# Kernel tuning notes

Hardware: AMD Instinct MI355X
Metric: run time of the kernel (lower is better)

## Reference

```python
import jax, jax.numpy as jnp
import numpy as np

OUT_NPOINT = 1024
NSAMPLE = 64
RADIUS = 0.32
BN_EPS = 1e-5


def _fps_single(pts, npoint):
    # pts: [N,3] -> indices [npoint], sequential furthest point sampling (starts at index 0,
    # matching pointnet2's furthest_point_sample with dists initialized to 1e10).
    N = pts.shape[0]

    def step(carry, _):
        mind, last = carry
        d = jnp.sum((pts - pts[last]) ** 2, axis=-1)  # [N]
        mind = jnp.minimum(mind, d)
        nxt = jnp.argmax(mind).astype(jnp.int32)
        return (mind, nxt), last

    init = (jnp.full((N,), 1e10, dtype=pts.dtype), jnp.int32(0))
    (_, _), idxs = jax.lax.scan(step, init, None, length=npoint)
    return idxs  # [npoint]


def _ball_query(xyz, new_xyz, radius, nsample):
    # xyz: [B,N,3], new_xyz: [B,M,3] -> idx [B,M,nsample] (first nsample in-ball points,
    # padded with the first found index, matching pointnet2 ball_query semantics).
    N = xyz.shape[1]
    d2 = jnp.sum((new_xyz[:, :, None, :] - xyz[:, None, :, :]) ** 2, axis=-1)  # [B,M,N]
    inball = d2 < radius * radius
    key = jnp.where(inball, jnp.arange(N, dtype=jnp.int32)[None, None, :], jnp.int32(N))
    sorted_keys = jnp.sort(key, axis=-1)[..., :nsample]  # [B,M,nsample]
    valid = sorted_keys < N
    first = jnp.where(sorted_keys[..., 0:1] < N, sorted_keys[..., 0:1], 0)
    return jnp.where(valid, sorted_keys, first)


def _group(features, idx):
    # features: [B,C,N], idx: [B,M,S] -> [B,C,M,S]
    return jax.vmap(lambda f, i: f[:, i])(features, idx)


def setup_inputs() -> dict:
    key = jax.random.key(0)
    ks = jax.random.split(key, 8)
    B, N, Cin, Cout = 8, 4096, 128, 256
    xyz = jax.random.uniform(ks[0], (B, N, 3), dtype=jnp.float32)
    features = jax.random.normal(ks[1], (B, Cin, N), dtype=jnp.float32)
    W = jax.random.normal(ks[2], (Cout, Cin), dtype=jnp.float32) * 0.05  # 1x1 conv weight
    b = jax.random.normal(ks[3], (Cout,), dtype=jnp.float32) * 0.05
    gamma = jax.random.uniform(ks[4], (Cout,), minval=0.5, maxval=1.5, dtype=jnp.float32)
    beta = jax.random.normal(ks[5], (Cout,), dtype=jnp.float32) * 0.1
    run_mean = jax.random.normal(ks[6], (Cout,), dtype=jnp.float32) * 0.1
    run_var = jax.random.uniform(ks[7], (Cout,), minval=0.5, maxval=1.5, dtype=jnp.float32)
    return {"xyz": xyz, "features": features, "W": W, "b": b,
            "gamma": gamma, "beta": beta, "run_mean": run_mean, "run_var": run_var}


def reference(xyz, features, W, b, gamma, beta, run_mean, run_var):
    # FPS to pick OUT_NPOINT centers
    fps_idx = jax.vmap(lambda p: _fps_single(p, OUT_NPOINT))(xyz)          # [B,M]
    new_xyz = jnp.take_along_axis(xyz, fps_idx[:, :, None], axis=1)        # [B,M,3]
    # ball-query neighbor indices and gather features (use_xyz=False)
    idx = _ball_query(xyz, new_xyz, RADIUS, NSAMPLE)                        # [B,M,S]
    grouped = _group(features, idx)                                         # [B,Cin,M,S]
    # pointwise conv (1x1) + BN (inference mode) + ReLU
    out = jnp.einsum('oc,bcms->boms', W, grouped) + b[None, :, None, None]  # [B,Cout,M,S]
    inv = jax.lax.rsqrt(run_var + BN_EPS)
    out = (out - run_mean[None, :, None, None]) * (gamma * inv)[None, :, None, None] + beta[None, :, None, None]
    out = jax.nn.relu(out)
    # max-pool over the neighbor axis
    return jnp.max(out, axis=-1)  # [B,Cout,M]
```

## Files before the change

kernel.cpp:

```cpp
#include <hip/hip_runtime.h>

#define N_PTS 4096
#define B_SZ  8
#define M_OUT 1024
#define NS    64
#define CIN   128
#define COUT  256
#define NW    496

typedef float v2f __attribute__((ext_vector_type(2)));

__device__ __forceinline__ float dpp_max_f32(float v) {
  int x = __builtin_bit_cast(int, v);
#define STG(C)                                                              \
  {                                                                         \
    int y = __builtin_amdgcn_update_dpp(x, x, C, 0xF, 0xF, false);          \
    float a = __builtin_bit_cast(float, x);                                 \
    float b2 = __builtin_bit_cast(float, y);                                \
    a = fmaxf(a, b2);                                                       \
    x = __builtin_bit_cast(int, a);                                         \
  }
  STG(0x111) STG(0x112) STG(0x114) STG(0x118) STG(0x142) STG(0x143)
#undef STG
  return __builtin_bit_cast(float, __builtin_amdgcn_readlane(x, 63));
}

__global__ __launch_bounds__(256) void fused_kernel(
    const float* __restrict__ xyz, int* __restrict__ fps_idx,
    int* __restrict__ gdone, const float* __restrict__ F,
    const float* __restrict__ W, float* __restrict__ Z,
    const float* __restrict__ bias, const float* __restrict__ gamma,
    const float* __restrict__ beta, const float* __restrict__ rmean,
    const float* __restrict__ rvar, float* __restrict__ out) {
  __shared__ __align__(16) float smem[13360];
  if (blockIdx.x < 8) {
#pragma clang fp contract(off)
    __builtin_amdgcn_s_setprio(3);
    float* lx = smem;
    float* ly = smem + 4096;
    float* lz = smem + 8192;
    float4 (*sl)[4] = (float4(*)[4])(smem + 12288);
    int (*siw)[4] = (int(*)[4])(smem + 12320);
    const int b = blockIdx.x, t = threadIdx.x;
    const int lane = t & 63, wv = t >> 6;
    const float* base = xyz + b * N_PTS * 3;
    for (int e = t; e < N_PTS; e += 256) {
      lx[e] = base[e * 3 + 0];
      ly[e] = base[e * 3 + 1];
      lz[e] = base[e * 3 + 2];
    }
    __syncthreads();
    const int nb = t * 16;
    v2f px[8], py[8], pz[8], m2[8];
#pragma unroll
    for (int j = 0; j < 8; ++j) {
      int n0 = nb + 2 * j;
      px[j] = (v2f){lx[n0], lx[n0 + 1]};
      py[j] = (v2f){ly[n0], ly[n0 + 1]};
      pz[j] = (v2f){lz[n0], lz[n0 + 1]};
      m2[j] = (v2f){1e10f, 1e10f};
    }
    int cur = 0;
    float cx = lx[0], cy = ly[0], cz = lz[0];
    for (int i = 0; i < M_OUT; ++i) {
      if (t == 0)
        __hip_atomic_store(fps_idx + b * M_OUT + i, cur, __ATOMIC_RELAXED,
                           __HIP_MEMORY_SCOPE_AGENT);
      float bv = -1.0f;
      int bj = 0;
#pragma unroll
      for (int j = 0; j < 8; ++j) {
        v2f dx = px[j] - cx, dy = py[j] - cy, dz = pz[j] - cz;
        v2f d = dx * dx + dy * dy;
        d = d + dz * dz;
        v2f md = __builtin_elementwise_min(m2[j], d);
        m2[j] = md;
        if (md.x > bv) { bv = md.x; bj = 2 * j; }
        if (md.y > bv) { bv = md.y; bj = 2 * j + 1; }
      }
      const float mv = dpp_max_f32(bv);
      unsigned long long tied = __ballot(bv == mv);
      const int fl = __ffsll(tied) - 1;
      const int bi = nb + bj;
      const int widx = __builtin_amdgcn_readlane(bi, fl);
      const float wx = lx[widx], wy = ly[widx], wz = lz[widx];
      const int p = i & 1;
      if (lane == 0) {
        sl[p][wv] = make_float4(mv, wx, wy, wz);
        siw[p][wv] = widx;
      }
      __syncthreads();
      float4 s0 = sl[p][0], s1 = sl[p][1], s2 = sl[p][2], s3 = sl[p][3];
      int i0 = siw[p][0], i1 = siw[p][1], i2 = siw[p][2], i3 = siw[p][3];
      float gv = s0.x, gx = s0.y, gy = s0.z, gz = s0.w;
      int gi = i0;
      bool bt;
      bt = (s1.x > gv) || (s1.x == gv && i1 < gi);
      if (bt) { gv = s1.x; gi = i1; gx = s1.y; gy = s1.z; gz = s1.w; }
      bt = (s2.x > gv) || (s2.x == gv && i2 < gi);
      if (bt) { gv = s2.x; gi = i2; gx = s2.y; gy = s2.z; gz = s2.w; }
      bt = (s3.x > gv) || (s3.x == gv && i3 < gi);
      if (bt) { gv = s3.x; gi = i3; gx = s3.y; gy = s3.z; gz = s3.w; }
      cur = gi; cx = gx; cy = gy; cz = gz;
    }
  } else {
    const int w = blockIdx.x - 8;
    {
      float (*Bs)[68] = (float(*)[68])smem;
      float (*As)[68] = (float(*)[68])(smem + 8704);
      const int tid = threadIdx.x;
      const int tx = tid & 15, ty = tid >> 4;
      for (int tile = w; tile < 2048; tile += NW) {
        __syncthreads();
        const int n0 = (tile & 63) * 64;
        const int o0 = ((tile >> 6) & 3) * 64;
        const int bb = tile >> 8;
        for (int l = 0; l < 32; ++l) {
          int e = l * 256 + tid;
          int c = e & 127, oo = e >> 7;
          Bs[c][oo] = W[(o0 + oo) * CIN + c];
        }
        float acc[4][4] = {};
        const float* Fb = F + bb * CIN * N_PTS;
        for (int c0 = 0; c0 < CIN; c0 += 32) {
          __syncthreads();
          for (int l = 0; l < 8; ++l) {
            int e = l * 256 + tid;
            int nn = e & 63, cc = e >> 6;
            As[cc][nn] = Fb[(c0 + cc) * N_PTS + n0 + nn];
          }
          __syncthreads();
#pragma unroll
          for (int cc = 0; cc < 32; ++cc) {
            float4 a = *(const float4*)&As[cc][tx * 4];
            float4 w4 = *(const float4*)&Bs[c0 + cc][ty * 4];
            acc[0][0] += a.x * w4.x; acc[0][1] += a.x * w4.y; acc[0][2] += a.x * w4.z; acc[0][3] += a.x * w4.w;
            acc[1][0] += a.y * w4.x; acc[1][1] += a.y * w4.y; acc[1][2] += a.y * w4.z; acc[1][3] += a.y * w4.w;
            acc[2][0] += a.z * w4.x; acc[2][1] += a.z * w4.y; acc[2][2] += a.z * w4.z; acc[2][3] += a.z * w4.w;
            acc[3][0] += a.w * w4.x; acc[3][1] += a.w * w4.y; acc[3][2] += a.w * w4.z; acc[3][3] += a.w * w4.w;
          }
        }
        float* Zb = Z + (size_t)(bb * N_PTS + n0) * COUT + o0;
#pragma unroll
        for (int i2 = 0; i2 < 4; ++i2) {
          int nn = tx * 4 + i2;
          float4 v = make_float4(acc[i2][0], acc[i2][1], acc[i2][2], acc[i2][3]);
          *(float4*)&Zb[(size_t)nn * COUT + ty * 4] = v;
        }
      }
    }
    __syncthreads();
    if (threadIdx.x == 0)
      __hip_atomic_fetch_add(gdone, 1, __ATOMIC_RELEASE,
                             __HIP_MEMORY_SCOPE_AGENT);
    if (threadIdx.x == 0) {
      while (__hip_atomic_load(gdone, __ATOMIC_ACQUIRE,
                               __HIP_MEMORY_SCOPE_AGENT) < NW)
        __builtin_amdgcn_s_sleep(16);
    }
    __syncthreads();
    __builtin_amdgcn_fence(__ATOMIC_ACQUIRE, "agent");
    const int lane = threadIdx.x & 63, wv = threadIdx.x >> 6;
    const int o = threadIdx.x;
    const float sc = gamma[o] * (1.0f / sqrtf(rvar[o] + 1e-5f));
    const float bo = bias[o], mo = rmean[o], bt = beta[o];
    float (*T)[9] = (float(*)[9])smem;
    int* sidx = (int*)(smem + 2304);
    int* cctr = (int*)(smem + 2816);
    for (int tb = w; tb < 1024; tb += NW) {
      const int b = tb & 7;
      const int m0 = (tb >> 3) * 8;
      if (threadIdx.x == 0) {
        int got;
        do {
          got = 1;
#pragma unroll
          for (int c = 0; c < 8; ++c) {
            int v = __hip_atomic_load(fps_idx + b * M_OUT + m0 + c,
                                      __ATOMIC_RELAXED,
                                      __HIP_MEMORY_SCOPE_AGENT);
            cctr[c] = v;
            got &= (v != -1);
          }
          if (!got) __builtin_amdgcn_s_sleep(8);
        } while (!got);
      }
      __syncthreads();
      const float* base = xyz + b * N_PTS * 3;
      {
#pragma clang fp contract(off)
        for (int c = wv; c < 8; c += 4) {
          const int cidx = cctr[c];
          const float cx = base[cidx * 3 + 0], cy = base[cidx * 3 + 1],
                      cz = base[cidx * 3 + 2];
          int* srow = sidx + c * NS;
          int cnt = 0, first = 0;
          for (int ch = 0; ch < N_PTS / 64 && cnt < NS; ++ch) {
            const int n = ch * 64 + lane;
            float dx = base[n * 3 + 0] - cx;
            float dy = base[n * 3 + 1] - cy;
            float dz = base[n * 3 + 2] - cz;
            float d = dx * dx + dy * dy;
            d = d + dz * dz;
            const bool inb = d < 0.1024f;
            unsigned long long mask = __ballot(inb);
            if (cnt == 0 && mask) first = ch * 64 + (__ffsll(mask) - 1);
            const int pos = cnt + __popcll(mask & ((1ull << lane) - 1ull));
            if (inb && pos < NS) srow[pos] = n;
            cnt += (int)__popcll(mask);
          }
          if (lane >= cnt) srow[lane] = first;
        }
      }
      __syncthreads();
      const float* Zb = Z + (size_t)b * N_PTS * COUT;
      for (int mi = 0; mi < 8; ++mi) {
        float c0 = -1e30f, c1 = -1e30f, c2 = -1e30f, c3 = -1e30f;
        float c4 = -1e30f, c5 = -1e30f, c6 = -1e30f, c7 = -1e30f;
#pragma unroll
        for (int s = 0; s < NS; s += 8) {
          int4 iv0 = *(const int4*)&sidx[mi * NS + s];
          int4 iv1 = *(const int4*)&sidx[mi * NS + s + 4];
          c0 = fmaxf(c0, Zb[(size_t)iv0.x * COUT + o]);
          c1 = fmaxf(c1, Zb[(size_t)iv0.y * COUT + o]);
          c2 = fmaxf(c2, Zb[(size_t)iv0.z * COUT + o]);
          c3 = fmaxf(c3, Zb[(size_t)iv0.w * COUT + o]);
          c4 = fmaxf(c4, Zb[(size_t)iv1.x * COUT + o]);
          c5 = fmaxf(c5, Zb[(size_t)iv1.y * COUT + o]);
          c6 = fmaxf(c6, Zb[(size_t)iv1.z * COUT + o]);
          c7 = fmaxf(c7, Zb[(size_t)iv1.w * COUT + o]);
        }
        float best = fmaxf(fmaxf(fmaxf(c0, c1), fmaxf(c2, c3)),
                           fmaxf(fmaxf(c4, c5), fmaxf(c6, c7)));
        float tv = best + bo;
        tv = (tv - mo) * sc + bt;
        T[o][mi] = fmaxf(tv, 0.0f);
      }
      __syncthreads();
      for (int l = 0; l < 8; ++l) {
        int e = l * 256 + (int)threadIdx.x;
        int mm = e & 7, oo = e >> 3;
        out[(size_t)(b * COUT + oo) * M_OUT + m0 + mm] = T[oo][mm];
      }
    }
  }
}

extern "C" void kernel_launch(void* const* d_in, const int* in_sizes, int n_in,
                              void* d_out, int out_size, void* d_ws, size_t ws_size,
                              hipStream_t stream) {
  const float* xyz      = (const float*)d_in[0];
  const float* features = (const float*)d_in[1];
  const float* W        = (const float*)d_in[2];
  const float* bias     = (const float*)d_in[3];
  const float* gamma    = (const float*)d_in[4];
  const float* beta     = (const float*)d_in[5];
  const float* rmean    = (const float*)d_in[6];
  const float* rvar     = (const float*)d_in[7];
  float* out = (float*)d_out;

  char* ws = (char*)d_ws;
  int* fps   = (int*)ws;
  int* flags = (int*)(ws + (48 << 10));
  float* Z   = (float*)(ws + (64 << 10) + (2 << 20));

  hipMemsetAsync(fps, 0xFF, 32 << 10, stream);
  hipMemsetAsync(flags, 0, 64, stream);
  fused_kernel<<<8 + NW, 256, 0, stream>>>(
      xyz, fps, flags, features, W, Z, bias, gamma, beta, rmean, rvar, out);
}
```

Baseline: 812.5 us.

## Split tail FPS centers into single-center tiles and merge memsets

Groups covering the last 64 FPS centers per batch are handled as single-center work items instead of 8-center tiles, so the ball-query and max-pool tail can follow the serial FPS loop more closely and finish sooner after the last index is published. The FPS loop exits after storing the final index, skipping the unused last distance update. The two workspace memsets are merged into one by initialising the done counter to -1 and waiting for NW-1. The per-center tail items use only one wave for the ball query and write output uncoalesced, adding some work-item overhead.

Result: no change. 803.0 us (-1.2%).

```diff
diff --git a/kernel.cpp b/kernel.cpp
--- a/kernel.cpp
+++ b/kernel.cpp
@@ -7,6 +7,8 @@
 #define CIN   128
 #define COUT  256
 #define NW    496
+#define NTILE_N 960
+#define NTILE_T 1472
 
 typedef float v2f __attribute__((ext_vector_type(2)));
 
@@ -66,6 +68,7 @@
       if (t == 0)
         __hip_atomic_store(fps_idx + b * M_OUT + i, cur, __ATOMIC_RELAXED,
                            __HIP_MEMORY_SCOPE_AGENT);
+      if (i == M_OUT - 1) break;
       float bv = -1.0f;
       int bj = 0;
 #pragma unroll
@@ -155,7 +158,7 @@
                              __HIP_MEMORY_SCOPE_AGENT);
     if (threadIdx.x == 0) {
       while (__hip_atomic_load(gdone, __ATOMIC_ACQUIRE,
-                               __HIP_MEMORY_SCOPE_AGENT) < NW)
+                               __HIP_MEMORY_SCOPE_AGENT) < NW - 1)
         __builtin_amdgcn_s_sleep(16);
     }
     __syncthreads();
@@ -167,33 +170,101 @@
     float (*T)[9] = (float(*)[9])smem;
     int* sidx = (int*)(smem + 2304);
     int* cctr = (int*)(smem + 2816);
-    for (int tb = w; tb < 1024; tb += NW) {
-      const int b = tb & 7;
-      const int m0 = (tb >> 3) * 8;
-      if (threadIdx.x == 0) {
-        int got;
-        do {
-          got = 1;
-#pragma unroll
-          for (int c = 0; c < 8; ++c) {
-            int v = __hip_atomic_load(fps_idx + b * M_OUT + m0 + c,
-                                      __ATOMIC_RELAXED,
-                                      __HIP_MEMORY_SCOPE_AGENT);
-            cctr[c] = v;
-            got &= (v != -1);
-          }
-          if (!got) __builtin_amdgcn_s_sleep(8);
-        } while (!got);
-      }
-      __syncthreads();
-      const float* base = xyz + b * N_PTS * 3;
-      {
+    for (int tb = w; tb < NTILE_T; tb += NW) {
+      if (tb < NTILE_N) {
+        const int b = tb & 7;
+        const int m0 = (tb >> 3) * 8;
+        if (threadIdx.x == 0) {
+          int got;
+          do {
+            got = 1;
+#pragma unroll
+            for (int c = 0; c < 8; ++c) {
+              int v = __hip_atomic_load(fps_idx + b * M_OUT + m0 + c,
+                                        __ATOMIC_RELAXED,
+                                        __HIP_MEMORY_SCOPE_AGENT);
+              cctr[c] = v;
+              got &= (v != -1);
+            }
+            if (!got) __builtin_amdgcn_s_sleep(8);
+          } while (!got);
+        }
+        __syncthreads();
+        const float* base = xyz + b * N_PTS * 3;
+        {
 #pragma clang fp contract(off)
-        for (int c = wv; c < 8; c += 4) {
-          const int cidx = cctr[c];
+          for (int c = wv; c < 8; c += 4) {
+            const int cidx = cctr[c];
+            const float cx = base[cidx * 3 + 0], cy = base[cidx * 3 + 1],
+                        cz = base[cidx * 3 + 2];
+            int* srow = sidx + c * NS;
+            int cnt = 0, first = 0;
+            for (int ch = 0; ch < N_PTS / 64 && cnt < NS; ++ch) {
+              const int n = ch * 64 + lane;
+              float dx = base[n * 3 + 0] - cx;
+              float dy = base[n * 3 + 1] - cy;
+              float dz = base[n * 3 + 2] - cz;
+              float d = dx * dx + dy * dy;
+              d = d + dz * dz;
+              const bool inb = d < 0.1024f;
+              unsigned long long mask = __ballot(inb);
+              if (cnt == 0 && mask) first = ch * 64 + (__ffsll(mask) - 1);
+              const int pos = cnt + __popcll(mask & ((1ull << lane) - 1ull));
+              if (inb && pos < NS) srow[pos] = n;
+              cnt += (int)__popcll(mask);
+            }
+            if (lane >= cnt) srow[lane] = first;
+          }
+        }
+        __syncthreads();
+        const float* Zb = Z + (size_t)b * N_PTS * COUT;
+        for (int mi = 0; mi < 8; ++mi) {
+          float c0 = -1e30f, c1 = -1e30f, c2 = -1e30f, c3 = -1e30f;
+          float c4 = -1e30f, c5 = -1e30f, c6 = -1e30f, c7 = -1e30f;
+#pragma unroll
+          for (int s = 0; s < NS; s += 8) {
+            int4 iv0 = *(const int4*)&sidx[mi * NS + s];
+            int4 iv1 = *(const int4*)&sidx[mi * NS + s + 4];
+            c0 = fmaxf(c0, Zb[(size_t)iv0.x * COUT + o]);
+            c1 = fmaxf(c1, Zb[(size_t)iv0.y * COUT + o]);
+            c2 = fmaxf(c2, Zb[(size_t)iv0.z * COUT + o]);
+            c3 = fmaxf(c3, Zb[(size_t)iv0.w * COUT + o]);
+            c4 = fmaxf(c4, Zb[(size_t)iv1.x * COUT + o]);
+            c5 = fmaxf(c5, Zb[(size_t)iv1.y * COUT + o]);
+            c6 = fmaxf(c6, Zb[(size_t)iv1.z * COUT + o]);
+            c7 = fmaxf(c7, Zb[(size_t)iv1.w * COUT + o]);
+          }
+          float best = fmaxf(fmaxf(fmaxf(c0, c1), fmaxf(c2, c3)),
+                             fmaxf(fmaxf(c4, c5), fmaxf(c6, c7)));
+          float tv = best + bo;
+          tv = (tv - mo) * sc + bt;
+          T[o][mi] = fmaxf(tv, 0.0f);
+        }
+        __syncthreads();
+        for (int l = 0; l < 8; ++l) {
+          int e = l * 256 + (int)threadIdx.x;
+          int mm = e & 7, oo = e >> 3;
+          out[(size_t)(b * COUT + oo) * M_OUT + m0 + mm] = T[oo][mm];
+        }
+      } else {
+        const int k = tb - NTILE_N;
+        const int b = k & 7;
+        const int m = 960 + (k >> 3);
+        if (threadIdx.x == 0) {
+          int v;
+          while ((v = __hip_atomic_load(fps_idx + b * M_OUT + m,
+                                        __ATOMIC_RELAXED,
+                                        __HIP_MEMORY_SCOPE_AGENT)) == -1)
+            __builtin_amdgcn_s_sleep(2);
+          cctr[0] = v;
+        }
+        __syncthreads();
+        const float* base = xyz + b * N_PTS * 3;
+        if (wv == 0) {
+#pragma clang fp contract(off)
+          const int cidx = cctr[0];
           const float cx = base[cidx * 3 + 0], cy = base[cidx * 3 + 1],
                       cz = base[cidx * 3 + 2];
-          int* srow = sidx + c * NS;
           int cnt = 0, first = 0;
           for (int ch = 0; ch < N_PTS / 64 && cnt < NS; ++ch) {
             const int n = ch * 64 + lane;
@@ -206,21 +277,19 @@
             unsigned long long mask = __ballot(inb);
             if (cnt == 0 && mask) first = ch * 64 + (__ffsll(mask) - 1);
             const int pos = cnt + __popcll(mask & ((1ull << lane) - 1ull));
-            if (inb && pos < NS) srow[pos] = n;
+            if (inb && pos < NS) sidx[pos] = n;
             cnt += (int)__popcll(mask);
           }
-          if (lane >= cnt) srow[lane] = first;
-        }
-      }
-      __syncthreads();
-      const float* Zb = Z + (size_t)b * N_PTS * COUT;
-      for (int mi = 0; mi < 8; ++mi) {
+          if (lane >= cnt) sidx[lane] = first;
+        }
+        __syncthreads();
+        const float* Zb = Z + (size_t)b * N_PTS * COUT;
         float c0 = -1e30f, c1 = -1e30f, c2 = -1e30f, c3 = -1e30f;
         float c4 = -1e30f, c5 = -1e30f, c6 = -1e30f, c7 = -1e30f;
 #pragma unroll
         for (int s = 0; s < NS; s += 8) {
-          int4 iv0 = *(const int4*)&sidx[mi * NS + s];
-          int4 iv1 = *(const int4*)&sidx[mi * NS + s + 4];
+          int4 iv0 = *(const int4*)&sidx[s];
+          int4 iv1 = *(const int4*)&sidx[s + 4];
           c0 = fmaxf(c0, Zb[(size_t)iv0.x * COUT + o]);
           c1 = fmaxf(c1, Zb[(size_t)iv0.y * COUT + o]);
           c2 = fmaxf(c2, Zb[(size_t)iv0.z * COUT + o]);
@@ -234,13 +303,7 @@
                            fmaxf(fmaxf(c4, c5), fmaxf(c6, c7)));
         float tv = best + bo;
         tv = (tv - mo) * sc + bt;
-        T[o][mi] = fmaxf(tv, 0.0f);
-      }
-      __syncthreads();
-      for (int l = 0; l < 8; ++l) {
-        int e = l * 256 + (int)threadIdx.x;
-        int mm = e & 7, oo = e >> 3;
-        out[(size_t)(b * COUT + oo) * M_OUT + m0 + mm] = T[oo][mm];
+        out[(size_t)(b * COUT + o) * M_OUT + m] = fmaxf(tv, 0.0f);
       }
     }
   }
@@ -261,11 +324,10 @@
 
   char* ws = (char*)d_ws;
   int* fps   = (int*)ws;
-  int* flags = (int*)(ws + (48 << 10));
+  int* gdone = (int*)(ws + (32 << 10));
   float* Z   = (float*)(ws + (64 << 10) + (2 << 20));
 
-  hipMemsetAsync(fps, 0xFF, 32 << 10, stream);
-  hipMemsetAsync(flags, 0, 64, stream);
+  hipMemsetAsync(ws, 0xFF, (32 << 10) + 64, stream);
   fused_kernel<<<8 + NW, 256, 0, stream>>>(
-      xyz, fps, flags, features, W, Z, bias, gamma, beta, rmean, rvar, out);
+      xyz, fps, gdone, features, W, Z, bias, gamma, beta, rmean, rvar, out);
 }
```
